# Performance work log

Hardware: AMD Instinct MI355X
Metric: run time of the kernel (lower is better)

## Reference

```python
import jax, jax.numpy as jnp
import numpy as np

D_HEADS = 2
MLP_H = 128
N_ENT = 100000
N_ROW = 30000
K_INST = 8
N_EDGE = 200000
N_REL = 200
IN_CH = 256
OUT_CH = 256


def _glorot(key, shape):
    fan_in = shape[0]
    return (jax.random.normal(key, shape, jnp.float32) / jnp.sqrt(jnp.float32(fan_in)))


def setup_inputs() -> dict:
    key = jax.random.key(0)
    ks = jax.random.split(key, 16)
    x = jax.random.normal(ks[0], (N_ENT, IN_CH), jnp.float32)
    ei0 = jax.random.randint(ks[1], (N_EDGE,), 0, N_ENT)   # target entities
    ei1 = jax.random.randint(ks[2], (N_EDGE,), 0, N_ROW)   # source instance rows
    edge_index = jnp.stack([ei0, ei1], 0).astype(jnp.int32)
    edge_order = jnp.arange(N_EDGE, dtype=jnp.int32)
    edge_type = jax.random.randint(ks[3], (N_EDGE,), 0, N_REL + 1).astype(jnp.int32)
    rel_embed = jax.random.normal(ks[4], (N_REL, IN_CH), jnp.float32)
    ids = jax.random.randint(ks[5], (N_ROW, K_INST), 0, N_ENT)
    pad = jax.random.uniform(ks[6], (N_ROW, K_INST)) < 0.4
    pad = pad.at[:, 0].set(False)  # each row keeps >=1 valid entry
    id2entity_instance = jnp.where(pad, -1, ids).astype(jnp.int32)
    return {
        'x': x, 'edge_index': edge_index, 'edge_order': edge_order,
        'edge_type': edge_type, 'rel_embed': rel_embed,
        'id2entity_instance': id2entity_instance,
        'W_in': _glorot(ks[7], (IN_CH, MLP_H * D_HEADS)), 'b_in': jnp.zeros((MLP_H * D_HEADS,), jnp.float32),
        'W_edge': _glorot(ks[8], (IN_CH, MLP_H * D_HEADS)), 'b_edge': jnp.zeros((MLP_H * D_HEADS,), jnp.float32),
        'W_sheaf': _glorot(ks[9], (2 * MLP_H, D_HEADS)), 'b_sheaf': jnp.zeros((D_HEADS,), jnp.float32),
        'W_conv': _glorot(ks[10], (MLP_H, MLP_H)), 'b_conv': jnp.zeros((MLP_H,), jnp.float32),
        'conv_bias': jnp.zeros((MLP_H,), jnp.float32),
        'w_rel': _glorot(ks[11], (IN_CH, OUT_CH)),
        'loop_rel': _glorot(ks[12], (1, IN_CH)),
        'mod_bias': jnp.zeros((OUT_CH,), jnp.float32),
        'bn_gamma': jnp.ones((OUT_CH,), jnp.float32), 'bn_beta': jnp.zeros((OUT_CH,), jnp.float32),
    }


def _forward(x, edge_index, edge_type, rel_embed, id2entity_instance,
             W_in, b_in, W_edge, b_edge, W_sheaf, b_sheaf,
             W_conv, b_conv, conv_bias, w_rel, loop_rel, mod_bias, bn_gamma, bn_beta):
    N, F = x.shape
    R = id2entity_instance.shape[0]
    E = edge_index.shape[1]
    d, H = D_HEADS, MLP_H
    # instance-dict embedding: padded gather (-1 wraps to the appended zero row) + masked mean
    x_add = jnp.concatenate([x, jnp.zeros((1, F), x.dtype)], 0)
    cnt = jnp.sum(id2entity_instance >= 0, axis=1, keepdims=True).astype(x.dtype)
    inst = jnp.sum(x_add[id2entity_instance], axis=1) / cnt          # (R, F)
    x_all = jnp.concatenate([x, inst], 0)                            # (N+R, F)
    Ntot = N + R
    # hypergraph incidence: each relational edge -> hyperedge with 2 nodes
    nodes = jnp.concatenate([edge_index[1] + N, edge_index[0]])      # (2E,)
    eids = jnp.concatenate([jnp.arange(E), jnp.arange(E)])           # (2E,)
    rel_full = jnp.concatenate([rel_embed, loop_rel], 0)             # (num_rels+1, F)
    # dual MLP projections (num_layers=1, InputNorm off -> plain linear)
    x_view = (x_all @ W_in + b_in).reshape(Ntot * d, H)
    e_view = (rel_full[edge_type] @ W_edge + b_edge).reshape(E * d, H)
    # sheaf builder (Diag, MLP_var1): mean over heads, gather, concat, linear, tanh
    x_mean = x_view.reshape(Ntot, d, H).mean(1)
    e_mean = e_view.reshape(E, d, H).mean(1)
    pair = jnp.concatenate([x_mean[nodes], e_mean[eids]], axis=-1)   # (2E, 2H)
    h_sheaf = jnp.tanh(pair @ W_sheaf + b_sheaf)                     # (2E, d)
    dr = jnp.arange(d)
    idx0 = (nodes[:, None] * d + dr).reshape(-1)                     # (2E*d,) node slots
    idx1 = (eids[:, None] * d + dr).reshape(-1)                      # (2E*d,) edge slots
    alpha = h_sheaf.reshape(-1)
    # HyperDiffusionDiagsheafConv (degree_norm, residual)
    h = x_view @ W_conv + b_conv                                     # (Ntot*d, H)
    Dn = jax.ops.segment_sum(alpha * alpha, idx0, num_segments=Ntot * d)
    Dinv = jnp.where(Dn > 0, 1.0 / Dn, 0.0)
    Be = jax.ops.segment_sum(jnp.ones_like(alpha), idx1, num_segments=E * d)
    Binv = jnp.where(Be > 0, 1.0 / Be, 0.0)
    ef = jax.ops.segment_sum((Binv[idx1] * alpha)[:, None] * h[idx0], idx1, num_segments=E * d)
    out = jax.ops.segment_sum((Dinv[idx0] * alpha)[:, None] * ef[idx1], idx0, num_segments=Ntot * d)
    out = out + conv_bias + h                                        # conv bias + residual
    out = jax.nn.elu(out).reshape(Ntot, d * H)
    out_ent = out[:N] + mod_bias
    # BatchNorm1d, training-mode statistics (biased var), eps=1e-5
    mu = out_ent.mean(0)
    var = out_ent.var(0)
    out_ent = (out_ent - mu) / jnp.sqrt(var + 1e-5) * bn_gamma + bn_beta
    r_out = (rel_full @ w_rel)[:-1]
    return out_ent, r_out


def reference(x, edge_index, edge_order, edge_type, rel_embed, id2entity_instance,
              W_in, b_in, W_edge, b_edge, W_sheaf, b_sheaf,
              W_conv, b_conv, conv_bias, w_rel, loop_rel, mod_bias, bn_gamma, bn_beta):
    # edge_order is accepted by the torch forward but unused
    return _forward(x, edge_index, edge_type, rel_embed, id2entity_instance,
                    W_in, b_in, W_edge, b_edge, W_sheaf, b_sheaf,
                    W_conv, b_conv, conv_bias, w_rel, loop_rel, mod_bias, bn_gamma, bn_beta)
```

## Files before the change

### kernel.cpp

```cpp
#include <hip/hip_runtime.h>
#include <stdint.h>

#define N_ENTC   100000
#define N_ROWC   30000
#define K_INSTC  8
#define N_EDGEC  200000
#define N_RELSC  200
#define NTOTC    (N_ENTC + N_ROWC)
#define CAPB     64

typedef _Float16 half8  __attribute__((ext_vector_type(8)));
typedef _Float16 half4v __attribute__((ext_vector_type(4)));
typedef float    float4v __attribute__((ext_vector_type(4)));

__global__ __launch_bounds__(256) void k_rel(
    const float* __restrict__ rel_embed, const float* __restrict__ loop_rel,
    const float* __restrict__ W_edge,    const float* __restrict__ b_edge,
    const float* __restrict__ W_sheaf,   const float* __restrict__ b_sheaf,
    const float* __restrict__ w_rel,
    float* __restrict__ s_edge_tab, float* __restrict__ out_rel)
{
  __shared__ float rel[256];
  __shared__ float eproj[256];
  __shared__ float em[128];
  int t = blockIdx.x;
  int c = threadIdx.x;
  rel[c] = (t < N_RELSC) ? rel_embed[t * 256 + c] : loop_rel[c];
  __syncthreads();
  float acc = b_edge[c];
  for (int k = 0; k < 256; ++k) acc += rel[k] * W_edge[k * 256 + c];
  eproj[c] = acc;
  __syncthreads();
  if (c < 128) em[c] = 0.5f * (eproj[c] + eproj[c + 128]);
  __syncthreads();
  if (c < 2) {
    float s = b_sheaf[c];
    for (int hh = 0; hh < 128; ++hh) s += em[hh] * W_sheaf[(128 + hh) * 2 + c];
    s_edge_tab[t * 2 + c] = s;
  }
  if (t < N_RELSC) {
    float ro = 0.f;
    for (int k = 0; k < 256; ++k) ro += rel[k] * w_rel[k * 256 + c];
    out_rel[t * 256 + c] = ro;
  }
}

__global__ __launch_bounds__(256) void k_fuse(
    const float* __restrict__ W_in,  const float* __restrict__ b_in,
    const float* __restrict__ W_conv, const float* __restrict__ b_conv,
    const float* __restrict__ W_sheaf,
    _Float16* __restrict__ Whi, _Float16* __restrict__ Wlo,
    float* __restrict__ b_comb, float* __restrict__ w_s)
{
  __shared__ float win[256];
  int k = blockIdx.x;
  int n = threadIdx.x;
  const float* src = (k < 256) ? (W_in + (size_t)k * 256) : b_in;
  win[n] = src[n];
  __syncthreads();
  int j = n >> 7, hh = n & 127;
  float acc = 0.f;
  for (int c = 0; c < 128; ++c)
    acc += win[j * 128 + c] * W_conv[c * 128 + hh];
  if (k < 256) {
    _Float16 hi = (_Float16)acc;
    _Float16 lo = (_Float16)(acc - (float)hi);
    int kt = k >> 5, g = (k >> 3) & 3, e = k & 7;
    int idx = ((kt * 16 + (n >> 4)) * 64 + (g * 16 + (n & 15))) * 8 + e;
    Whi[idx] = hi; Wlo[idx] = lo;
    if (n < 2) {
      float s = 0.f;
      for (int c2 = 0; c2 < 128; ++c2)
        s += 0.5f * (win[c2] + win[c2 + 128]) * W_sheaf[c2 * 2 + n];
      w_s[k * 2 + n] = s;
    }
  } else {
    b_comb[n] = acc + b_conv[hh];
    if (n < 2) {
      float s = 0.f;
      for (int c2 = 0; c2 < 128; ++c2)
        s += 0.5f * (win[c2] + win[c2 + 128]) * W_sheaf[c2 * 2 + n];
      w_s[512 + n] = s;
    }
  }
}

__global__ __launch_bounds__(256) void k_inst(
    const float* __restrict__ x, const int* __restrict__ ids,
    float* __restrict__ inst)
{
  int tid = threadIdx.x;
  int r = blockIdx.x * 4 + (tid >> 6);
  int ch = (tid & 63) * 4;
  if (r >= N_ROWC) return;
  float4 s = make_float4(0.f, 0.f, 0.f, 0.f);
  int cnt = 0;
#pragma unroll
  for (int k = 0; k < K_INSTC; ++k) {
    int id = ids[r * K_INSTC + k];
    if (id >= 0) {
      float4 v = *(const float4*)(x + (size_t)id * 256 + ch);
      s.x += v.x; s.y += v.y; s.z += v.z; s.w += v.w;
      cnt++;
    }
  }
  float inv = 1.f / (float)cnt;
  float4 o; o.x = s.x * inv; o.y = s.y * inv; o.z = s.z * inv; o.w = s.w * inv;
  *(float4*)(inst + (size_t)r * 256 + ch) = o;
}

__global__ __launch_bounds__(256) void k_snode(
    const float* __restrict__ x, const float* __restrict__ inst,
    const float* __restrict__ w_s, float* __restrict__ s_node)
{
  __shared__ float ws[514];
  int tid = threadIdx.x;
  for (int i = tid; i < 514; i += 256) ws[i] = w_s[i];
  __syncthreads();
  int r = tid >> 2, q = tid & 3;
  int row = blockIdx.x * 64 + r;
  if (row >= NTOTC) return;
  const float* src = (row < N_ENTC) ? (x + (size_t)row * 256)
                                    : (inst + (size_t)(row - N_ENTC) * 256);
  float s0 = 0.f, s1 = 0.f;
  int kbase = q * 64;
#pragma unroll
  for (int i = 0; i < 16; ++i) {
    float4 v = *(const float4*)(src + kbase + i * 4);
    int k2 = (kbase + i * 4) * 2;
    s0 += v.x * ws[k2 + 0] + v.y * ws[k2 + 2] + v.z * ws[k2 + 4] + v.w * ws[k2 + 6];
    s1 += v.x * ws[k2 + 1] + v.y * ws[k2 + 3] + v.z * ws[k2 + 5] + v.w * ws[k2 + 7];
  }
  s0 += __shfl_xor(s0, 1); s0 += __shfl_xor(s0, 2);
  s1 += __shfl_xor(s1, 1); s1 += __shfl_xor(s1, 2);
  if (q < 2) {
    float val = (q == 0) ? s0 : s1;
    s_node[(size_t)row * 2 + q] = val + ws[512 + q];
  }
}

__global__ __launch_bounds__(256, 3) void k_gemm(
    const float* __restrict__ x, const float* __restrict__ inst,
    const _Float16* __restrict__ Whi, const _Float16* __restrict__ Wlo,
    const float* __restrict__ b_comb,
    float* __restrict__ h)
{
  __shared__ _Float16 Ahi[64 * 64];
  __shared__ _Float16 Alo[64 * 64];

  int tid = threadIdx.x;
  int l = tid & 63;
  int w = tid >> 6;
  int row0 = blockIdx.x * 64;
  int g = l >> 4;
  int cn = l & 15;

  float4v acc[4][4];
#pragma unroll
  for (int a = 0; a < 4; ++a)
#pragma unroll
    for (int b = 0; b < 4; ++b) acc[a][b] = (float4v)(0.f);

  int rs = tid >> 4;
  int kb = (tid & 15) * 4;

  for (int ks = 0; ks < 4; ++ks) {
    int k0 = ks * 64;
#pragma unroll
    for (int i = 0; i < 4; ++i) {
      int r = rs + i * 16;
      int row = row0 + r;
      float4 v = make_float4(0.f, 0.f, 0.f, 0.f);
      if (row < N_ENTC) {
        v = *(const float4*)(x + (size_t)row * 256 + k0 + kb);
      } else if (row < NTOTC) {
        v = *(const float4*)(inst + (size_t)(row - N_ENTC) * 256 + k0 + kb);
      }
      half4v hv, lv;
      hv[0] = (_Float16)v.x; lv[0] = (_Float16)(v.x - (float)hv[0]);
      hv[1] = (_Float16)v.y; lv[1] = (_Float16)(v.y - (float)hv[1]);
      hv[2] = (_Float16)v.z; lv[2] = (_Float16)(v.z - (float)hv[2]);
      hv[3] = (_Float16)v.w; lv[3] = (_Float16)(v.w - (float)hv[3]);
      int idx = r * 64 + (((kb >> 3) ^ (r & 7)) << 3) + (kb & 7);
      *(half4v*)&Ahi[idx] = hv;
      *(half4v*)&Alo[idx] = lv;
    }
    __syncthreads();
#pragma unroll
    for (int kf = 0; kf < 2; ++kf) {
      int kt = ks * 2 + kf;
      half8 ah[4], al[4];
#pragma unroll
      for (int mt = 0; mt < 4; ++mt) {
        int row = mt * 16 + cn;
        int slot = (kf * 4 + g) ^ (cn & 7);
        int aidx = row * 64 + slot * 8;
        ah[mt] = *(const half8*)&Ahi[aidx];
        al[mt] = *(const half8*)&Alo[aidx];
      }
#pragma unroll
      for (int nt = 0; nt < 4; ++nt) {
        size_t boff = ((size_t)(kt * 16 + w * 4 + nt) * 64 + l) * 8;
        half8 bh = *(const half8*)(Whi + boff);
        half8 bl = *(const half8*)(Wlo + boff);
#pragma unroll
        for (int mt = 0; mt < 4; ++mt) {
          acc[mt][nt] = __builtin_amdgcn_mfma_f32_16x16x32_f16(ah[mt], bh, acc[mt][nt], 0, 0, 0);
          acc[mt][nt] = __builtin_amdgcn_mfma_f32_16x16x32_f16(al[mt], bh, acc[mt][nt], 0, 0, 0);
          acc[mt][nt] = __builtin_amdgcn_mfma_f32_16x16x32_f16(ah[mt], bl, acc[mt][nt], 0, 0, 0);
        }
      }
    }
    __syncthreads();
  }
#pragma unroll
  for (int nt = 0; nt < 4; ++nt) {
    int col = w * 64 + nt * 16 + cn;
    float bc = b_comb[col];
#pragma unroll
    for (int mt = 0; mt < 4; ++mt) {
      int rbase = row0 + mt * 16 + g * 4;
#pragma unroll
      for (int rr = 0; rr < 4; ++rr) {
        int row = rbase + rr;
        if (row < NTOTC)
          h[(size_t)row * 256 + col] = acc[mt][nt][rr] + bc;
      }
    }
  }
}

__global__ __launch_bounds__(256) void k_alpha(
    const int* __restrict__ ei0, const int* __restrict__ ei1,
    const int* __restrict__ etype,
    const float* __restrict__ s_node, const float* __restrict__ s_edge_tab,
    float* __restrict__ Dn, int* __restrict__ cnt,
    int4* __restrict__ bE)
{
  int e = blockIdx.x * 256 + threadIdx.x;
  if (e >= N_EDGEC) return;
  int t = ei0[e], rI = ei1[e], ty = etype[e];
  float se0 = s_edge_tab[ty * 2 + 0], se1 = s_edge_tab[ty * 2 + 1];
  const float* snI = &s_node[(size_t)(N_ENTC + rI) * 2];
  const float* snT = &s_node[(size_t)t * 2];
  float a10 = tanhf(snI[0] + se0);
  float a11 = tanhf(snI[1] + se1);
  float a20 = tanhf(snT[0] + se0);
  float a21 = tanhf(snT[1] + se1);
  atomicAdd(&Dn[t * 2 + 0], a20 * a20);
  atomicAdd(&Dn[t * 2 + 1], a21 * a21);
  int pos = atomicAdd(&cnt[t], 1);
  if (pos < CAPB) {
    int4 ee;
    ee.x = rI; ee.y = 0;
    ee.z = __float_as_int(0.5f * a10 * a20);
    ee.w = __float_as_int(0.5f * a11 * a21);
    bE[(size_t)t * CAPB + pos] = ee;
  }
}

#define EPB 64
__global__ __launch_bounds__(256) void k_gather(
    float* h, const float* __restrict__ Dn,
    const int* __restrict__ cnt, const int4* __restrict__ bE,
    const float* __restrict__ conv_bias, const float* __restrict__ mod_bias,
    double* __restrict__ bnacc)
{
  __shared__ double red[4][512];
  int tid = threadIdx.x;
  int wv = tid >> 6, l = tid & 63;
  int ch = l * 4;
  int j = l >> 5;
  float4 cb = *(const float4*)(conv_bias + (ch & 127));
  float4 mb = *(const float4*)(mod_bias + ch);
  double s0 = 0, s1 = 0, s2 = 0, s3 = 0;
  double q0 = 0, q1 = 0, q2 = 0, q3 = 0;
  int tbase = blockIdx.x * EPB + wv * (EPB / 4);
  for (int i = 0; i < EPB / 4; ++i) {
    int t = tbase + i;
    if (t >= N_ENTC) break;
    int deg = cnt[t]; deg = (deg < CAPB) ? deg : CAPB;
    float dn = Dn[t * 2 + j];
    float dinv = (dn > 0.f) ? (1.0f / dn) : 0.f;
    float sf = (dn > 0.f) ? 1.5f : 1.0f;
    float4 cr = make_float4(0.f, 0.f, 0.f, 0.f);
    const int4* be = bE + (size_t)t * CAPB;
    for (int k = 0; k < deg; ++k) {
      int4 ee = be[k];
      float c = (l < 32) ? __int_as_float(ee.z) : __int_as_float(ee.w);
      float4 hv = *(const float4*)(h + (size_t)(N_ENTC + ee.x) * 256 + ch);
      cr.x += c * hv.x; cr.y += c * hv.y; cr.z += c * hv.z; cr.w += c * hv.w;
    }
    size_t idx = (size_t)t * 256 + ch;
    float4 ht = *(const float4*)(h + idx);
    float4 o;
    o.x = dinv * cr.x + sf * ht.x + cb.x;
    o.y = dinv * cr.y + sf * ht.y + cb.y;
    o.z = dinv * cr.z + sf * ht.z + cb.z;
    o.w = dinv * cr.w + sf * ht.w + cb.w;
    o.x = (o.x > 0.f) ? o.x : expm1f(o.x);
    o.y = (o.y > 0.f) ? o.y : expm1f(o.y);
    o.z = (o.z > 0.f) ? o.z : expm1f(o.z);
    o.w = (o.w > 0.f) ? o.w : expm1f(o.w);
    o.x += mb.x; o.y += mb.y; o.z += mb.z; o.w += mb.w;
    *(float4*)(h + idx) = o;
    s0 += (double)o.x; q0 += (double)o.x * (double)o.x;
    s1 += (double)o.y; q1 += (double)o.y * (double)o.y;
    s2 += (double)o.z; q2 += (double)o.z * (double)o.z;
    s3 += (double)o.w; q3 += (double)o.w * (double)o.w;
  }
  red[wv][ch + 0] = s0; red[wv][ch + 1] = s1;
  red[wv][ch + 2] = s2; red[wv][ch + 3] = s3;
  red[wv][256 + ch + 0] = q0; red[wv][256 + ch + 1] = q1;
  red[wv][256 + ch + 2] = q2; red[wv][256 + ch + 3] = q3;
  __syncthreads();
  double ssum = red[0][tid] + red[1][tid] + red[2][tid] + red[3][tid];
  double qsum = red[0][256 + tid] + red[1][256 + tid]
              + red[2][256 + tid] + red[3][256 + tid];
  atomicAdd(&bnacc[tid], ssum);
  atomicAdd(&bnacc[256 + tid], qsum);
}

__global__ void k_bnstat(const double* __restrict__ bnacc,
                         const float* __restrict__ gamma, const float* __restrict__ beta,
                         float* __restrict__ ss)
{
  int c = threadIdx.x;
  double mu  = bnacc[c] / (double)N_ENTC;
  double var = bnacc[256 + c] / (double)N_ENTC - mu * mu;
  double istd = 1.0 / sqrt(var + 1e-5);
  float sc = (float)((double)gamma[c] * istd);
  float sh = (float)((double)beta[c] - mu * (double)sc);
  ss[c] = sc; ss[256 + c] = sh;
}

__global__ __launch_bounds__(256) void k_store(
    const float* __restrict__ prebn, const float* __restrict__ ss,
    float* __restrict__ out)
{
  size_t stride = (size_t)gridDim.x * 256 * 4;
  for (size_t i = ((size_t)blockIdx.x * 256 + threadIdx.x) * 4;
       i < (size_t)N_ENTC * 256; i += stride) {
    float4 a = *(const float4*)(prebn + i);
    int c = (int)(i & 255);
    float4 o;
    o.x = a.x * ss[c + 0] + ss[256 + c + 0];
    o.y = a.y * ss[c + 1] + ss[256 + c + 1];
    o.z = a.z * ss[c + 2] + ss[256 + c + 2];
    o.w = a.w * ss[c + 3] + ss[256 + c + 3];
    *(float4*)(out + i) = o;
  }
}

extern "C" void kernel_launch(void* const* d_in, const int* in_sizes, int n_in,
                              void* d_out, int out_size, void* d_ws, size_t ws_size,
                              hipStream_t stream)
{
  (void)in_sizes; (void)n_in; (void)out_size; (void)ws_size;

  const float* x         = (const float*)d_in[0];
  const int*   edge_idx  = (const int*)d_in[1];
  const int*   etype     = (const int*)d_in[3];
  const float* rel_embed = (const float*)d_in[4];
  const int*   ids       = (const int*)d_in[5];
  const float* W_in      = (const float*)d_in[6];
  const float* b_in      = (const float*)d_in[7];
  const float* W_edge    = (const float*)d_in[8];
  const float* b_edge    = (const float*)d_in[9];
  const float* W_sheaf   = (const float*)d_in[10];
  const float* b_sheaf   = (const float*)d_in[11];
  const float* W_conv    = (const float*)d_in[12];
  const float* b_conv    = (const float*)d_in[13];
  const float* conv_bias = (const float*)d_in[14];
  const float* w_rel     = (const float*)d_in[15];
  const float* loop_rel  = (const float*)d_in[16];
  const float* mod_bias  = (const float*)d_in[17];
  const float* bn_gamma  = (const float*)d_in[18];
  const float* bn_beta   = (const float*)d_in[19];

  const int* ei0 = edge_idx;
  const int* ei1 = edge_idx + N_EDGEC;

  char* ws = (char*)d_ws;
  const size_t OFF_H     = 0;
  const size_t OFF_DN    = OFF_H     + (size_t)NTOTC * 256 * 4;
  const size_t OFF_BN    = OFF_DN    + (size_t)N_ENTC * 2 * 4;
  const size_t OFF_CNT   = OFF_BN    + 4096;
  const size_t OFF_SNODE = OFF_CNT   + (size_t)N_ENTC * 4;
  const size_t OFF_SS    = OFF_SNODE + (size_t)NTOTC * 2 * 4;
  const size_t OFF_SEDGE = OFF_SS    + 2048;
  const size_t OFF_BIG   = OFF_SEDGE + 2048;
  const size_t OFF_WHI   = OFF_BIG   + (size_t)N_ROWC * 256 * 4;
  const size_t OFF_WLO   = OFF_WHI   + 131072;
  const size_t OFF_BC    = OFF_WLO   + 131072;
  const size_t OFF_WS    = OFF_BC    + 1024;
  const size_t OFF_BE    = OFF_BIG;

  float*     h       = (float*)(ws + OFF_H);
  float*     Dn      = (float*)(ws + OFF_DN);
  double*    bnacc   = (double*)(ws + OFF_BN);
  int*       cnt     = (int*)(ws + OFF_CNT);
  float*     s_node  = (float*)(ws + OFF_SNODE);
  float*     ss      = (float*)(ws + OFF_SS);
  float*     s_edge  = (float*)(ws + OFF_SEDGE);
  float*     inst    = (float*)(ws + OFF_BIG);
  _Float16*  Whi     = (_Float16*)(ws + OFF_WHI);
  _Float16*  Wlo     = (_Float16*)(ws + OFF_WLO);
  float*     b_comb  = (float*)(ws + OFF_BC);
  float*     w_s     = (float*)(ws + OFF_WS);
  int4*      bE      = (int4*)(ws + OFF_BE);

  float* out_ent = (float*)d_out;
  float* out_rel = (float*)d_out + (size_t)N_ENTC * 256;

  hipMemsetAsync(ws + OFF_DN, 0,
                 (size_t)N_ENTC * 2 * 4 + 4096 + (size_t)N_ENTC * 4, stream);

  k_rel<<<201, 256, 0, stream>>>(rel_embed, loop_rel, W_edge, b_edge,
                                 W_sheaf, b_sheaf, w_rel, s_edge, out_rel);
  k_fuse<<<257, 256, 0, stream>>>(W_in, b_in, W_conv, b_conv, W_sheaf,
                                  Whi, Wlo, b_comb, w_s);
  k_inst<<<(N_ROWC + 3) / 4, 256, 0, stream>>>(x, ids, inst);
  k_snode<<<(NTOTC + 63) / 64, 256, 0, stream>>>(x, inst, w_s, s_node);
  k_gemm<<<(NTOTC + 63) / 64, 256, 0, stream>>>(x, inst, Whi, Wlo, b_comb, h);

  k_alpha<<<(N_EDGEC + 255) / 256, 256, 0, stream>>>(ei0, ei1, etype,
                                                     s_node, s_edge,
                                                     Dn, cnt, bE);
  k_gather<<<(N_ENTC + EPB - 1) / EPB, 256, 0, stream>>>(h, Dn, cnt, bE,
                                                         conv_bias, mod_bias,
                                                         bnacc);
  k_bnstat<<<1, 256, 0, stream>>>(bnacc, bn_gamma, bn_beta, ss);
  k_store<<<8192, 256, 0, stream>>>(h, ss, out_ent);
}
```

Measured before the change: 541.3 us.

## Run GEMM on entities only and derive instance rows by averaging outputs

Because the instance rows are means of entity rows and the projection is linear with a bias, the GEMM and node-score projection now run only on the 100k entity rows. A new kernel averages the already projected h rows and s_node values to produce the instance rows. The node-score dot product is fused into the GEMM load loop, and the GEMM epilogue stages results through LDS so rows are written as coalesced float4 stores. The gather kernel also processes fewer targets per block. This removes the separate inst and snode passes and cuts GEMM work by about a quarter. Summing outputs instead of inputs changes floating-point rounding slightly.

```diff
diff --git a/kernel.cpp b/kernel.cpp
--- a/kernel.cpp
+++ b/kernel.cpp
@@ -85,70 +85,22 @@
   }
 }
 
-__global__ __launch_bounds__(256) void k_inst(
-    const float* __restrict__ x, const int* __restrict__ ids,
-    float* __restrict__ inst)
-{
+__global__ __launch_bounds__(256, 3) void k_gemm(
+    const float* __restrict__ x,
+    const _Float16* __restrict__ Whi, const _Float16* __restrict__ Wlo,
+    const float* __restrict__ b_comb, const float* __restrict__ w_s,
+    float* __restrict__ h, float* __restrict__ s_node)
+{
+  __shared__ union {
+    struct { _Float16 Ahi[64 * 64]; _Float16 Alo[64 * 64]; } a;
+    float ep[16 * 256];
+  } sm;
+  __shared__ float wsl[514];
+
   int tid = threadIdx.x;
-  int r = blockIdx.x * 4 + (tid >> 6);
-  int ch = (tid & 63) * 4;
-  if (r >= N_ROWC) return;
-  float4 s = make_float4(0.f, 0.f, 0.f, 0.f);
-  int cnt = 0;
-#pragma unroll
-  for (int k = 0; k < K_INSTC; ++k) {
-    int id = ids[r * K_INSTC + k];
-    if (id >= 0) {
-      float4 v = *(const float4*)(x + (size_t)id * 256 + ch);
-      s.x += v.x; s.y += v.y; s.z += v.z; s.w += v.w;
-      cnt++;
-    }
-  }
-  float inv = 1.f / (float)cnt;
-  float4 o; o.x = s.x * inv; o.y = s.y * inv; o.z = s.z * inv; o.w = s.w * inv;
-  *(float4*)(inst + (size_t)r * 256 + ch) = o;
-}
-
-__global__ __launch_bounds__(256) void k_snode(
-    const float* __restrict__ x, const float* __restrict__ inst,
-    const float* __restrict__ w_s, float* __restrict__ s_node)
-{
-  __shared__ float ws[514];
-  int tid = threadIdx.x;
-  for (int i = tid; i < 514; i += 256) ws[i] = w_s[i];
-  __syncthreads();
-  int r = tid >> 2, q = tid & 3;
-  int row = blockIdx.x * 64 + r;
-  if (row >= NTOTC) return;
-  const float* src = (row < N_ENTC) ? (x + (size_t)row * 256)
-                                    : (inst + (size_t)(row - N_ENTC) * 256);
-  float s0 = 0.f, s1 = 0.f;
-  int kbase = q * 64;
-#pragma unroll
-  for (int i = 0; i < 16; ++i) {
-    float4 v = *(const float4*)(src + kbase + i * 4);
-    int k2 = (kbase + i * 4) * 2;
-    s0 += v.x * ws[k2 + 0] + v.y * ws[k2 + 2] + v.z * ws[k2 + 4] + v.w * ws[k2 + 6];
-    s1 += v.x * ws[k2 + 1] + v.y * ws[k2 + 3] + v.z * ws[k2 + 5] + v.w * ws[k2 + 7];
-  }
-  s0 += __shfl_xor(s0, 1); s0 += __shfl_xor(s0, 2);
-  s1 += __shfl_xor(s1, 1); s1 += __shfl_xor(s1, 2);
-  if (q < 2) {
-    float val = (q == 0) ? s0 : s1;
-    s_node[(size_t)row * 2 + q] = val + ws[512 + q];
-  }
-}
-
-__global__ __launch_bounds__(256, 3) void k_gemm(
-    const float* __restrict__ x, const float* __restrict__ inst,
-    const _Float16* __restrict__ Whi, const _Float16* __restrict__ Wlo,
-    const float* __restrict__ b_comb,
-    float* __restrict__ h)
-{
-  __shared__ _Float16 Ahi[64 * 64];
-  __shared__ _Float16 Alo[64 * 64];
-
-  int tid = threadIdx.x;
+  for (int i = tid; i < 514; i += 256) wsl[i] = w_s[i];
+  __syncthreads();
+
   int l = tid & 63;
   int w = tid >> 6;
   int row0 = blockIdx.x * 64;
@@ -163,6 +115,9 @@
 
   int rs = tid >> 4;
   int kb = (tid & 15) * 4;
+  float sn0[4], sn1[4];
+#pragma unroll
+  for (int i = 0; i < 4; ++i) { sn0[i] = 0.f; sn1[i] = 0.f; }
 
   for (int ks = 0; ks < 4; ++ks) {
     int k0 = ks * 64;
@@ -173,17 +128,20 @@
       float4 v = make_float4(0.f, 0.f, 0.f, 0.f);
       if (row < N_ENTC) {
         v = *(const float4*)(x + (size_t)row * 256 + k0 + kb);
-      } else if (row < NTOTC) {
-        v = *(const float4*)(inst + (size_t)(row - N_ENTC) * 256 + k0 + kb);
       }
+      int k2 = (k0 + kb) * 2;
+      sn0[i] += v.x * wsl[k2 + 0] + v.y * wsl[k2 + 2]
+              + v.z * wsl[k2 + 4] + v.w * wsl[k2 + 6];
+      sn1[i] += v.x * wsl[k2 + 1] + v.y * wsl[k2 + 3]
+              + v.z * wsl[k2 + 5] + v.w * wsl[k2 + 7];
       half4v hv, lv;
       hv[0] = (_Float16)v.x; lv[0] = (_Float16)(v.x - (float)hv[0]);
       hv[1] = (_Float16)v.y; lv[1] = (_Float16)(v.y - (float)hv[1]);
       hv[2] = (_Float16)v.z; lv[2] = (_Float16)(v.z - (float)hv[2]);
       hv[3] = (_Float16)v.w; lv[3] = (_Float16)(v.w - (float)hv[3]);
       int idx = r * 64 + (((kb >> 3) ^ (r & 7)) << 3) + (kb & 7);
-      *(half4v*)&Ahi[idx] = hv;
-      *(half4v*)&Alo[idx] = lv;
+      *(half4v*)&sm.a.Ahi[idx] = hv;
+      *(half4v*)&sm.a.Alo[idx] = lv;
     }
     __syncthreads();
 #pragma unroll
@@ -195,8 +153,8 @@
         int row = mt * 16 + cn;
         int slot = (kf * 4 + g) ^ (cn & 7);
         int aidx = row * 64 + slot * 8;
-        ah[mt] = *(const half8*)&Ahi[aidx];
-        al[mt] = *(const half8*)&Alo[aidx];
+        ah[mt] = *(const half8*)&sm.a.Ahi[aidx];
+        al[mt] = *(const half8*)&sm.a.Alo[aidx];
       }
 #pragma unroll
       for (int nt = 0; nt < 4; ++nt) {
@@ -213,20 +171,83 @@
     }
     __syncthreads();
   }
-#pragma unroll
-  for (int nt = 0; nt < 4; ++nt) {
-    int col = w * 64 + nt * 16 + cn;
-    float bc = b_comb[col];
-#pragma unroll
-    for (int mt = 0; mt < 4; ++mt) {
-      int rbase = row0 + mt * 16 + g * 4;
+
+#pragma unroll
+  for (int i = 0; i < 4; ++i) {
+    float a0 = sn0[i], a1 = sn1[i];
+#pragma unroll
+    for (int m = 1; m <= 8; m <<= 1) {
+      a0 += __shfl_xor(a0, m);
+      a1 += __shfl_xor(a1, m);
+    }
+    int row = row0 + rs + i * 16;
+    if ((tid & 15) == 0 && row < N_ENTC) {
+      s_node[(size_t)row * 2 + 0] = a0 + wsl[512];
+      s_node[(size_t)row * 2 + 1] = a1 + wsl[513];
+    }
+  }
+
+  float bc[4];
+#pragma unroll
+  for (int nt = 0; nt < 4; ++nt) bc[nt] = b_comb[w * 64 + nt * 16 + cn];
+#pragma unroll
+  for (int mt = 0; mt < 4; ++mt) {
+    __syncthreads();
+#pragma unroll
+    for (int nt = 0; nt < 4; ++nt)
 #pragma unroll
       for (int rr = 0; rr < 4; ++rr) {
-        int row = rbase + rr;
-        if (row < NTOTC)
-          h[(size_t)row * 256 + col] = acc[mt][nt][rr] + bc;
+        int row = g * 4 + rr;
+        int col = w * 64 + nt * 16 + cn;
+        int colp = col ^ (g << 4);
+        sm.ep[row * 256 + colp] = acc[mt][nt][rr] + bc[nt];
       }
-    }
+    __syncthreads();
+    int gr = row0 + mt * 16;
+#pragma unroll
+    for (int q = 0; q < 4; ++q) {
+      int f = tid + q * 256;
+      int row = f >> 6, c4 = (f & 63) * 4;
+      int colp = c4 ^ (((row >> 2) & 3) << 4);
+      float4 vv = *(float4*)&sm.ep[row * 256 + colp];
+      int grow = gr + row;
+      if (grow < N_ENTC)
+        *(float4*)&h[(size_t)grow * 256 + c4] = vv;
+    }
+  }
+}
+
+__global__ __launch_bounds__(256) void k_hinst(
+    float* __restrict__ h, float* __restrict__ s_node,
+    const int* __restrict__ ids)
+{
+  int tid = threadIdx.x;
+  int r = blockIdx.x * 4 + (tid >> 6);
+  int l = tid & 63;
+  int ch = l * 4;
+  if (r >= N_ROWC) return;
+  float4 s = make_float4(0.f, 0.f, 0.f, 0.f);
+  float sn0 = 0.f, sn1 = 0.f;
+  int cnt = 0;
+#pragma unroll
+  for (int k = 0; k < K_INSTC; ++k) {
+    int id = ids[r * K_INSTC + k];
+    if (id >= 0) {
+      float4 v = *(const float4*)(h + (size_t)id * 256 + ch);
+      s.x += v.x; s.y += v.y; s.z += v.z; s.w += v.w;
+      if (l == 0) {
+        sn0 += s_node[(size_t)id * 2 + 0];
+        sn1 += s_node[(size_t)id * 2 + 1];
+      }
+      cnt++;
+    }
+  }
+  float inv = 1.f / (float)cnt;
+  float4 o; o.x = s.x * inv; o.y = s.y * inv; o.z = s.z * inv; o.w = s.w * inv;
+  *(float4*)(h + (size_t)(N_ENTC + r) * 256 + ch) = o;
+  if (l == 0) {
+    s_node[(size_t)(N_ENTC + r) * 2 + 0] = sn0 * inv;
+    s_node[(size_t)(N_ENTC + r) * 2 + 1] = sn1 * inv;
   }
 }
 
@@ -259,7 +280,7 @@
   }
 }
 
-#define EPB 64
+#define EPB 32
 __global__ __launch_bounds__(256) void k_gather(
     float* h, const float* __restrict__ Dn,
     const int* __restrict__ cnt, const int4* __restrict__ bE,
@@ -403,7 +424,6 @@
   float*     s_node  = (float*)(ws + OFF_SNODE);
   float*     ss      = (float*)(ws + OFF_SS);
   float*     s_edge  = (float*)(ws + OFF_SEDGE);
-  float*     inst    = (float*)(ws + OFF_BIG);
   _Float16*  Whi     = (_Float16*)(ws + OFF_WHI);
   _Float16*  Wlo     = (_Float16*)(ws + OFF_WLO);
   float*     b_comb  = (float*)(ws + OFF_BC);
@@ -420,9 +440,9 @@
                                  W_sheaf, b_sheaf, w_rel, s_edge, out_rel);
   k_fuse<<<257, 256, 0, stream>>>(W_in, b_in, W_conv, b_conv, W_sheaf,
                                   Whi, Wlo, b_comb, w_s);
-  k_inst<<<(N_ROWC + 3) / 4, 256, 0, stream>>>(x, ids, inst);
-  k_snode<<<(NTOTC + 63) / 64, 256, 0, stream>>>(x, inst, w_s, s_node);
-  k_gemm<<<(NTOTC + 63) / 64, 256, 0, stream>>>(x, inst, Whi, Wlo, b_comb, h);
+  k_gemm<<<(N_ENTC + 63) / 64, 256, 0, stream>>>(x, Whi, Wlo, b_comb, w_s,
+                                                 h, s_node);
+  k_hinst<<<(N_ROWC + 3) / 4, 256, 0, stream>>>(h, s_node, ids);
 
   k_alpha<<<(N_EDGEC + 255) / 256, 256, 0, stream>>>(ei0, ei1, etype,
                                                      s_node, s_edge,
```

After: 614.3 us. +13.5%, slower.

## Compute instance rows by averaging projected entity features after the GEMM

Applied to the files above, without the earlier changes.

Because the input projection is linear, the instance rows of h and s_node are now formed by averaging the already-projected entity rows instead of averaging raw x and then projecting. This removes the inst buffer, its write and re-read, and 30000 rows of GEMM and s_node work. The cost is a gather kernel reading h after the GEMM, and bias is included correctly only because each average has weights summing to one. The gather kernel's entities-per-block is also halved to give more blocks.

```diff
diff --git a/kernel.cpp b/kernel.cpp
--- a/kernel.cpp
+++ b/kernel.cpp
@@ -85,32 +85,8 @@
   }
 }
 
-__global__ __launch_bounds__(256) void k_inst(
-    const float* __restrict__ x, const int* __restrict__ ids,
-    float* __restrict__ inst)
-{
-  int tid = threadIdx.x;
-  int r = blockIdx.x * 4 + (tid >> 6);
-  int ch = (tid & 63) * 4;
-  if (r >= N_ROWC) return;
-  float4 s = make_float4(0.f, 0.f, 0.f, 0.f);
-  int cnt = 0;
-#pragma unroll
-  for (int k = 0; k < K_INSTC; ++k) {
-    int id = ids[r * K_INSTC + k];
-    if (id >= 0) {
-      float4 v = *(const float4*)(x + (size_t)id * 256 + ch);
-      s.x += v.x; s.y += v.y; s.z += v.z; s.w += v.w;
-      cnt++;
-    }
-  }
-  float inv = 1.f / (float)cnt;
-  float4 o; o.x = s.x * inv; o.y = s.y * inv; o.z = s.z * inv; o.w = s.w * inv;
-  *(float4*)(inst + (size_t)r * 256 + ch) = o;
-}
-
 __global__ __launch_bounds__(256) void k_snode(
-    const float* __restrict__ x, const float* __restrict__ inst,
+    const float* __restrict__ x,
     const float* __restrict__ w_s, float* __restrict__ s_node)
 {
   __shared__ float ws[514];
@@ -119,9 +95,8 @@
   __syncthreads();
   int r = tid >> 2, q = tid & 3;
   int row = blockIdx.x * 64 + r;
-  if (row >= NTOTC) return;
-  const float* src = (row < N_ENTC) ? (x + (size_t)row * 256)
-                                    : (inst + (size_t)(row - N_ENTC) * 256);
+  if (row >= N_ENTC) return;
+  const float* src = x + (size_t)row * 256;
   float s0 = 0.f, s1 = 0.f;
   int kbase = q * 64;
 #pragma unroll
@@ -140,7 +115,7 @@
 }
 
 __global__ __launch_bounds__(256, 3) void k_gemm(
-    const float* __restrict__ x, const float* __restrict__ inst,
+    const float* __restrict__ x,
     const _Float16* __restrict__ Whi, const _Float16* __restrict__ Wlo,
     const float* __restrict__ b_comb,
     float* __restrict__ h)
@@ -173,8 +148,6 @@
       float4 v = make_float4(0.f, 0.f, 0.f, 0.f);
       if (row < N_ENTC) {
         v = *(const float4*)(x + (size_t)row * 256 + k0 + kb);
-      } else if (row < NTOTC) {
-        v = *(const float4*)(inst + (size_t)(row - N_ENTC) * 256 + k0 + kb);
       }
       half4v hv, lv;
       hv[0] = (_Float16)v.x; lv[0] = (_Float16)(v.x - (float)hv[0]);
@@ -223,10 +196,44 @@
 #pragma unroll
       for (int rr = 0; rr < 4; ++rr) {
         int row = rbase + rr;
-        if (row < NTOTC)
+        if (row < N_ENTC)
           h[(size_t)row * 256 + col] = acc[mt][nt][rr] + bc;
       }
     }
+  }
+}
+
+__global__ __launch_bounds__(256) void k_hinst(
+    float* __restrict__ h, float* __restrict__ s_node,
+    const int* __restrict__ ids)
+{
+  int tid = threadIdx.x;
+  int r = blockIdx.x * 4 + (tid >> 6);
+  int l = tid & 63;
+  int ch = l * 4;
+  if (r >= N_ROWC) return;
+  float4 s = make_float4(0.f, 0.f, 0.f, 0.f);
+  float sn0 = 0.f, sn1 = 0.f;
+  int cnt = 0;
+#pragma unroll
+  for (int k = 0; k < K_INSTC; ++k) {
+    int id = ids[r * K_INSTC + k];
+    if (id >= 0) {
+      float4 v = *(const float4*)(h + (size_t)id * 256 + ch);
+      s.x += v.x; s.y += v.y; s.z += v.z; s.w += v.w;
+      if (l == 0) {
+        sn0 += s_node[(size_t)id * 2 + 0];
+        sn1 += s_node[(size_t)id * 2 + 1];
+      }
+      cnt++;
+    }
+  }
+  float inv = 1.f / (float)cnt;
+  float4 o; o.x = s.x * inv; o.y = s.y * inv; o.z = s.z * inv; o.w = s.w * inv;
+  *(float4*)(h + (size_t)(N_ENTC + r) * 256 + ch) = o;
+  if (l == 0) {
+    s_node[(size_t)(N_ENTC + r) * 2 + 0] = sn0 * inv;
+    s_node[(size_t)(N_ENTC + r) * 2 + 1] = sn1 * inv;
   }
 }
 
@@ -259,7 +266,7 @@
   }
 }
 
-#define EPB 64
+#define EPB 32
 __global__ __launch_bounds__(256) void k_gather(
     float* h, const float* __restrict__ Dn,
     const int* __restrict__ cnt, const int4* __restrict__ bE,
@@ -403,7 +410,6 @@
   float*     s_node  = (float*)(ws + OFF_SNODE);
   float*     ss      = (float*)(ws + OFF_SS);
   float*     s_edge  = (float*)(ws + OFF_SEDGE);
-  float*     inst    = (float*)(ws + OFF_BIG);
   _Float16*  Whi     = (_Float16*)(ws + OFF_WHI);
   _Float16*  Wlo     = (_Float16*)(ws + OFF_WLO);
   float*     b_comb  = (float*)(ws + OFF_BC);
@@ -420,9 +426,9 @@
                                  W_sheaf, b_sheaf, w_rel, s_edge, out_rel);
   k_fuse<<<257, 256, 0, stream>>>(W_in, b_in, W_conv, b_conv, W_sheaf,
                                   Whi, Wlo, b_comb, w_s);
-  k_inst<<<(N_ROWC + 3) / 4, 256, 0, stream>>>(x, ids, inst);
-  k_snode<<<(NTOTC + 63) / 64, 256, 0, stream>>>(x, inst, w_s, s_node);
-  k_gemm<<<(NTOTC + 63) / 64, 256, 0, stream>>>(x, inst, Whi, Wlo, b_comb, h);
+  k_snode<<<(N_ENTC + 63) / 64, 256, 0, stream>>>(x, w_s, s_node);
+  k_gemm<<<(N_ENTC + 63) / 64, 256, 0, stream>>>(x, Whi, Wlo, b_comb, h);
+  k_hinst<<<(N_ROWC + 3) / 4, 256, 0, stream>>>(h, s_node, ids);
 
   k_alpha<<<(N_EDGEC + 255) / 256, 256, 0, stream>>>(ei0, ei1, etype,
                                                      s_node, s_edge,
```

Result: no change. 537.4 us (-0.7%).
